# Kernel tuning notes

Measured on AMD Instinct MI355X. Metric: run time of the kernel, lower is better.

Reference implementation:

```python
import jax, jax.numpy as jnp
import numpy as np

B, L = 2, 256
CHAR, WORD = 8000, 50000
CE, WE, HID, REL = 128, 128, 256, 24
IN_DIM = CE + WE


def _lstm(x, mask, W, U, b):
    # Keras LSTM cell: z = x@W + h@U + b split into (i,f,g,o); masked steps carry state through.
    # x: (B, T, D) float, mask: (B, T) bool
    h0 = jnp.zeros((x.shape[0], U.shape[0]), x.dtype)

    def step(carry, xm):
        h, c = carry
        xt, mt = xm
        z = xt @ W + h @ U + b
        i, f, g, o = jnp.split(z, 4, axis=-1)
        c_new = jax.nn.sigmoid(f) * c + jax.nn.sigmoid(i) * jnp.tanh(g)
        h_new = jax.nn.sigmoid(o) * jnp.tanh(c_new)
        m = mt[:, None]
        h2 = jnp.where(m, h_new, h)
        c2 = jnp.where(m, c_new, c)
        return (h2, c2), h2

    _, hs = jax.lax.scan(step, (h0, h0), (jnp.swapaxes(x, 0, 1), jnp.swapaxes(mask, 0, 1)))
    return jnp.swapaxes(hs, 0, 1)  # (B, T, HID)


def _head(enc, Wu, bu, Wv, bv, Wuv, buv, Wc, bc):
    # Original: tile relu(u) over axis 1 (depends on j) and relu(v) over axis 2 (depends on i),
    # concat -> Dense. Equivalent fused form: split Wuv and broadcast-add the two projections.
    u = jax.nn.relu(enc @ Wu + bu)  # (B, L, E)
    v = jax.nn.relu(enc @ Wv + bv)  # (B, L, E)
    E = Wu.shape[1]
    uv = (jnp.einsum('bjd,de->bje', u, Wuv[:E])[:, None, :, :]
          + jnp.einsum('bid,de->bie', v, Wuv[E:])[:, :, None, :]
          + buv)  # (B, L, L, E)
    return uv @ Wc + bc  # (B, L, L, out)


def setup_inputs() -> dict:
    key = jax.random.key(0)
    ks = jax.random.split(key, 64)

    def w(k, shape):
        return jax.random.normal(k, shape, jnp.float32) * 0.05

    inp = {
        'inputs': jax.random.randint(ks[0], (B, L), 0, CHAR, jnp.int32),
        'input_words': jax.random.randint(ks[1], (B, L), 0, WORD, jnp.int32),
        'input_max_len': L,
        'embed_table': w(ks[2], (CHAR, CE)),
        'word_embed_table': w(ks[3], (WORD, WE)),
        'lstm_fwd_W': w(ks[4], (IN_DIM, 4 * HID)),
        'lstm_fwd_U': w(ks[5], (HID, 4 * HID)),
        'lstm_fwd_b': jnp.zeros((4 * HID,), jnp.float32),
        'lstm_bwd_W': w(ks[6], (IN_DIM, 4 * HID)),
        'lstm_bwd_U': w(ks[7], (HID, 4 * HID)),
        'lstm_bwd_b': jnp.zeros((4 * HID,), jnp.float32),
    }
    i = 8
    for name, out in (('eh', 1), ('hh', REL), ('tt', REL)):
        inp[f'{name}_u_W'] = w(ks[i], (2 * HID, CE)); i += 1
        inp[f'{name}_u_b'] = jnp.zeros((CE,), jnp.float32)
        inp[f'{name}_v_W'] = w(ks[i], (2 * HID, CE)); i += 1
        inp[f'{name}_v_b'] = jnp.zeros((CE,), jnp.float32)
        inp[f'{name}_uv_W'] = w(ks[i], (2 * CE, CE)); i += 1
        inp[f'{name}_uv_b'] = jnp.zeros((CE,), jnp.float32)
        inp[f'{name}_cls_W'] = w(ks[i], (CE, out)); i += 1
        inp[f'{name}_cls_b'] = jnp.zeros((out,), jnp.float32)
    return inp


def reference(inputs, input_words, input_max_len, embed_table, word_embed_table,
              lstm_fwd_W, lstm_fwd_U, lstm_fwd_b, lstm_bwd_W, lstm_bwd_U, lstm_bwd_b,
              eh_u_W, eh_u_b, eh_v_W, eh_v_b, eh_uv_W, eh_uv_b, eh_cls_W, eh_cls_b,
              hh_u_W, hh_u_b, hh_v_W, hh_v_b, hh_uv_W, hh_uv_b, hh_cls_W, hh_cls_b,
              tt_u_W, tt_u_b, tt_v_W, tt_v_b, tt_uv_W, tt_uv_b, tt_cls_W, tt_cls_b):
    mask = inputs != 0  # (B, L)
    x = jnp.concatenate([embed_table[inputs], word_embed_table[input_words]], axis=-1)
    h_fwd = _lstm(x, mask, lstm_fwd_W, lstm_fwd_U, lstm_fwd_b)
    h_bwd = _lstm(x[:, ::-1], mask[:, ::-1], lstm_bwd_W, lstm_bwd_U, lstm_bwd_b)[:, ::-1]
    enc = jnp.concatenate([h_fwd, h_bwd], axis=-1)  # (B, L, 2*HID)
    eh = jax.nn.sigmoid(_head(enc, eh_u_W, eh_u_b, eh_v_W, eh_v_b, eh_uv_W, eh_uv_b, eh_cls_W, eh_cls_b))
    hh = jax.nn.softmax(_head(enc, hh_u_W, hh_u_b, hh_v_W, hh_v_b, hh_uv_W, hh_uv_b, hh_cls_W, hh_cls_b), axis=-1)
    tt = jax.nn.softmax(_head(enc, tt_u_W, tt_u_b, tt_v_W, tt_v_b, tt_uv_W, tt_uv_b, tt_cls_W, tt_cls_b), axis=-1)
    return (eh, hh, tt)
```

## Files before the change

### kernel.cpp

```cpp
#include <hip/hip_runtime.h>
#include <hip/hip_bf16.h>

typedef unsigned short u16;
typedef unsigned int u32;
typedef unsigned long long u64;

#define LSEQ 256

constexpr int XW_F  = 0;
constexpr int XW_B  = 524288;
constexpr int HF_O  = 1048576;
constexpr int HB_O  = 1179648;
constexpr int PEH_O = 1703936;
constexpr int QEH_O = 1704448;
constexpr int PHH_O = 1704960;
constexpr int QHH_O = 1717248;
constexpr int PTT_O = 1729536;
constexpr int QTT_O = 1741824;

constexpr u64 SENT64 = 0x7FC000007FC00000ULL;

__device__ __forceinline__ float b2f(u16 u) {
  u32 x = ((u32)u) << 16; float f;
  __builtin_memcpy(&f, &x, 4); return f;
}
__device__ __forceinline__ u16 f2b(float f) {
  u32 x; __builtin_memcpy(&x, &f, 4);
  u32 r = (x + 0x7fffu + ((x >> 16) & 1u)) >> 16;
  return (u16)r;
}
__device__ __forceinline__ float sigm(float x) {
  return __builtin_amdgcn_rcpf(1.f + __expf(-x));
}
__device__ __forceinline__ float tanh_fast(float x) {
  return 2.f * __builtin_amdgcn_rcpf(1.f + __expf(-2.f * x)) - 1.f;
}
__device__ __forceinline__ u64 aload64(u64* p) {
  return __hip_atomic_load(p, __ATOMIC_RELAXED, __HIP_MEMORY_SCOPE_AGENT);
}
__device__ __forceinline__ void astore64(u64* p, u64 v) {
  __hip_atomic_store(p, v, __ATOMIC_RELAXED, __HIP_MEMORY_SCOPE_AGENT);
}
__device__ __forceinline__ bool detect_f32(const void* etab) {
  u32 w = ((const u32*)etab)[threadIdx.x & 63];
  u64 m = __ballot((w & 0x4000u) != 0);
  return __popcll(m) >= 16;
}
__device__ __forceinline__ float ldf(const void* p, int i, bool f32m) {
  return f32m ? ((const float*)p)[i] : b2f(((const u16*)p)[i]);
}

__global__ __launch_bounds__(256) void k_embed_xw(
    const int* __restrict__ toks, const int* __restrict__ wrds,
    const void* __restrict__ etab, const void* __restrict__ wtab,
    const void* __restrict__ Wf, const void* __restrict__ bf_,
    const void* __restrict__ Wb, const void* __restrict__ bb_,
    float* __restrict__ ws)
{
  __shared__ float xs[8][256];
  const int tid = threadIdx.x, bx = blockIdx.x;
  const int rg = bx >> 2, part = bx & 3, dir = part >> 1, ch = part & 1;
  {
    u64* hz = (u64*)(ws + HF_O) + (bx * 256 + tid) * 2;
    astore64(hz, SENT64); astore64(hz + 1, SENT64);
  }
  const bool f32m = detect_f32(etab);
  for (int rr = 0; rr < 8; rr++) {
    const int row = rg * 8 + rr;
    const int id = toks[row], wid = wrds[row];
    xs[rr][tid] = (tid < 128) ? ldf(etab, id * 128 + tid, f32m)
                              : ldf(wtab, wid * 128 + (tid - 128), f32m);
  }
  __syncthreads();
  const void* W = dir ? Wb : Wf;
  const void* bb = dir ? bb_ : bf_;
  const int c0 = ch * 512 + 2 * tid;
  float acc[8][2];
#pragma unroll
  for (int rr = 0; rr < 8; rr++) { acc[rr][0] = 0.f; acc[rr][1] = 0.f; }
  if (f32m) {
    const float2* W2 = (const float2*)W;
    for (int k = 0; k < 256; k++) {
      const float2 w = W2[k * 512 + (c0 >> 1)];
#pragma unroll
      for (int rr = 0; rr < 8; rr++) {
        const float x = xs[rr][k];
        acc[rr][0] = fmaf(x, w.x, acc[rr][0]);
        acc[rr][1] = fmaf(x, w.y, acc[rr][1]);
      }
    }
  } else {
    const u32* W2 = (const u32*)W;
    for (int k = 0; k < 256; k++) {
      const u32 v = W2[k * 512 + (c0 >> 1)];
      const float wx = b2f(v & 0xffff), wy = b2f(v >> 16);
#pragma unroll
      for (int rr = 0; rr < 8; rr++) {
        const float x = xs[rr][k];
        acc[rr][0] = fmaf(x, wx, acc[rr][0]);
        acc[rr][1] = fmaf(x, wy, acc[rr][1]);
      }
    }
  }
  const float b0 = ldf(bb, c0, f32m), b1 = ldf(bb, c0 + 1, f32m);
  float* xwb = ws + (dir ? XW_B : XW_F);
#pragma unroll
  for (int rr = 0; rr < 8; rr++) {
    const int row = rg * 8 + rr;
    float2 o = make_float2(acc[rr][0] + b0, acc[rr][1] + b1);
    *(float2*)(xwb + row * 1024 + c0) = o;
  }
}

__global__ __launch_bounds__(256, 1) void k_lstm(
    const int* __restrict__ toks,
    const void* __restrict__ Uf_raw, const void* __restrict__ Ub_raw,
    const void* __restrict__ etab, float* __restrict__ ws)
{
  __shared__ float2 hsh0[256], hsh1[256];
  __shared__ float psum0[8][128], psum1[8][128];
  __shared__ float zsh0[128], zsh1[128];
  __shared__ int msk[512];
  const int tid = threadIdx.x;
  const int w = blockIdx.x, base = w * 16;
  const int q = tid & 31, ksec = tid >> 5, k0 = ksec * 32;
  u64* h0 = (u64*)(ws + HF_O);
  u64* h1 = (u64*)(ws + HB_O);
  const float* xw0 = ws + XW_F;
  const float* xw1 = ws + XW_B;
  const bool f32m = detect_f32(etab);

  const int lc0 = 2 * q;
  const int gc0 = (lc0 >> 4) * 256 + base + (lc0 & 15);
  float2 us0[32], us1[32];
  if (f32m) {
    const float* U0 = (const float*)Uf_raw;
    const float* U1 = (const float*)Ub_raw;
#pragma unroll
    for (int j = 0; j < 32; j++) {
      us0[j] = *(const float2*)(U0 + (k0 + j) * 1024 + gc0);
      us1[j] = *(const float2*)(U1 + (k0 + j) * 1024 + gc0);
    }
  } else {
    const u32* U0 = (const u32*)Uf_raw;
    const u32* U1 = (const u32*)Ub_raw;
#pragma unroll
    for (int j = 0; j < 32; j++) {
      u32 v0 = U0[((k0 + j) * 1024 + gc0) >> 1];
      u32 v1 = U1[((k0 + j) * 1024 + gc0) >> 1];
      us0[j] = make_float2(b2f(v0 & 0xffff), b2f(v0 >> 16));
      us1[j] = make_float2(b2f(v1 & 0xffff), b2f(v1 >> 16));
    }
  }
  const int rlc = tid >> 1, rbb = tid & 1;
  const int rgc = (rlc >> 4) * 256 + base + (rlc & 15);
  const int gj = tid & 15, gb = (tid >> 4) & 1;
  const bool own = (tid >= base) && (tid < base + 16);

  msk[tid] = toks[tid]; msk[tid + 256] = toks[tid + 256];
  hsh0[tid] = make_float2(0.f, 0.f);
  hsh1[tid] = make_float2(0.f, 0.f);
  float c0Reg = 0.f, h0Reg = 0.f, c1Reg = 0.f, h1Reg = 0.f;
  float xw0reg = xw0[rbb * 262144 + 0 * 1024 + rgc];
  float xw1reg = xw1[rbb * 262144 + 255 * 1024 + rgc];
  __syncthreads();

  for (int s = 0; s < LSEQ; s++) {
    u64 v1 = 0;
    if (s > 0 && !own) v1 = aload64(&h1[(s - 1) * 256 + tid]);
    {
      float4 a = make_float4(0.f, 0.f, 0.f, 0.f);
#pragma unroll
      for (int j = 0; j < 32; j++) {
        const float2 h = hsh0[k0 + j];
        const float2 u = us0[j];
        a.x = fmaf(h.x, u.x, a.x); a.y = fmaf(h.y, u.x, a.y);
        a.z = fmaf(h.x, u.y, a.z); a.w = fmaf(h.y, u.y, a.w);
      }
      *(float4*)&psum0[ksec][4 * q] = a;
    }
    __syncthreads();
    if (tid < 128) {
      float z = xw0reg;
#pragma unroll
      for (int ks = 0; ks < 8; ks++) z += psum0[ks][tid];
      zsh0[tid] = z;
      const int t2 = (s < 255) ? s + 1 : 255;
      xw0reg = xw0[rbb * 262144 + t2 * 1024 + rgc];
    }
    __syncthreads();
    if (tid < 32) {
      const float zi = zsh0[gj * 2 + gb],        zf = zsh0[(16 + gj) * 2 + gb];
      const float zg = zsh0[(32 + gj) * 2 + gb], zo = zsh0[(48 + gj) * 2 + gb];
      const float cn = sigm(zf) * c0Reg + sigm(zi) * tanh_fast(zg);
      const float hn = sigm(zo) * tanh_fast(cn);
      if (msk[gb * 256 + s] != 0) { c0Reg = cn; h0Reg = hn; }
      const float hp = __shfl_xor(h0Reg, 16);
      if (tid < 16) {
        const float2 fv = make_float2(h0Reg, hp);
        hsh0[base + tid] = fv;
        u64 pv; __builtin_memcpy(&pv, &fv, 8);
        astore64(&h0[s * 256 + base + tid], pv);
      }
    }
    if (s > 0 && !own) {
      while (v1 == SENT64) v1 = aload64(&h1[(s - 1) * 256 + tid]);
      float2 hv; __builtin_memcpy(&hv, &v1, 8);
      hsh1[tid] = hv;
    }
    __syncthreads();
    u64 v0 = 0;
    if (s < 255 && !own) v0 = aload64(&h0[s * 256 + tid]);
    {
      float4 a = make_float4(0.f, 0.f, 0.f, 0.f);
#pragma unroll
      for (int j = 0; j < 32; j++) {
        const float2 h = hsh1[k0 + j];
        const float2 u = us1[j];
        a.x = fmaf(h.x, u.x, a.x); a.y = fmaf(h.y, u.x, a.y);
        a.z = fmaf(h.x, u.y, a.z); a.w = fmaf(h.y, u.y, a.w);
      }
      *(float4*)&psum1[ksec][4 * q] = a;
    }
    __syncthreads();
    if (tid < 128) {
      float z = xw1reg;
#pragma unroll
      for (int ks = 0; ks < 8; ks++) z += psum1[ks][tid];
      zsh1[tid] = z;
      const int t2 = (s < 255) ? 254 - s : 0;
      xw1reg = xw1[rbb * 262144 + t2 * 1024 + rgc];
    }
    __syncthreads();
    if (tid < 32) {
      const float zi = zsh1[gj * 2 + gb],        zf = zsh1[(16 + gj) * 2 + gb];
      const float zg = zsh1[(32 + gj) * 2 + gb], zo = zsh1[(48 + gj) * 2 + gb];
      const float cn = sigm(zf) * c1Reg + sigm(zi) * tanh_fast(zg);
      const float hn = sigm(zo) * tanh_fast(cn);
      if (msk[gb * 256 + (255 - s)] != 0) { c1Reg = cn; h1Reg = hn; }
      const float hp = __shfl_xor(h1Reg, 16);
      if (tid < 16) {
        const float2 fv = make_float2(h1Reg, hp);
        hsh1[base + tid] = fv;
        u64 pv; __builtin_memcpy(&pv, &fv, 8);
        astore64(&h1[s * 256 + base + tid], pv);
      }
    }
    if (s < 255 && !own) {
      while (v0 == SENT64) v0 = aload64(&h0[s * 256 + tid]);
      float2 hv; __builtin_memcpy(&hv, &v0, 8);
      hsh0[tid] = hv;
    }
    __syncthreads();
  }
}

struct HeadPack { const void* p[24]; };

__global__ __launch_bounds__(256) void k_uvpq(
    HeadPack pk, const void* __restrict__ etab, float* __restrict__ ws)
{
  __shared__ float encs_t[512][8];
  __shared__ float usv_t[2][128][8];
  __shared__ float apq[2][8][128];
  __shared__ float wc[3072];
  const int tid = threadIdx.x, rgp = blockIdx.x, hd = blockIdx.y;
  const bool f32m = detect_f32(etab);
  const void* uW  = pk.p[hd * 8 + 0]; const void* ub  = pk.p[hd * 8 + 1];
  const void* vW  = pk.p[hd * 8 + 2]; const void* vb  = pk.p[hd * 8 + 3];
  const void* uvW = pk.p[hd * 8 + 4]; const void* uvb = pk.p[hd * 8 + 5];
  const void* cW  = pk.p[hd * 8 + 6];
  const int nout = (hd == 0) ? 1 : 24;
  for (int i = tid; i < 128 * nout; i += 256) wc[i] = ldf(cW, i, f32m);
  for (int i = tid; i < 4096; i += 256) {
    const int h = i >> 3, rr = i & 7;
    const int row = rgp * 8 + rr, b = row >> 8, t = row & 255;
    encs_t[h][rr] = (h < 256)
        ? ws[HF_O + t * 512 + h * 2 + b]
        : ws[HB_O + (255 - t) * 512 + (h - 256) * 2 + b];
  }
  __syncthreads();
  {
    const int mat = tid >> 7, cs = tid & 127;
    const void* W = mat ? vW : uW;
    const float bias = ldf(mat ? vb : ub, cs, f32m);
    float acc[8];
#pragma unroll
    for (int rr = 0; rr < 8; rr++) acc[rr] = 0.f;
    if (f32m) {
      const float* Wf = (const float*)W;
      for (int k = 0; k < 512; k++) {
        const float wv = Wf[k * 128 + cs];
        const float4 e0 = *(const float4*)&encs_t[k][0];
        const float4 e1 = *(const float4*)&encs_t[k][4];
        acc[0] = fmaf(e0.x, wv, acc[0]); acc[1] = fmaf(e0.y, wv, acc[1]);
        acc[2] = fmaf(e0.z, wv, acc[2]); acc[3] = fmaf(e0.w, wv, acc[3]);
        acc[4] = fmaf(e1.x, wv, acc[4]); acc[5] = fmaf(e1.y, wv, acc[5]);
        acc[6] = fmaf(e1.z, wv, acc[6]); acc[7] = fmaf(e1.w, wv, acc[7]);
      }
    } else {
      const u16* Wf = (const u16*)W;
      for (int k = 0; k < 512; k++) {
        const float wv = b2f(Wf[k * 128 + cs]);
        const float4 e0 = *(const float4*)&encs_t[k][0];
        const float4 e1 = *(const float4*)&encs_t[k][4];
        acc[0] = fmaf(e0.x, wv, acc[0]); acc[1] = fmaf(e0.y, wv, acc[1]);
        acc[2] = fmaf(e0.z, wv, acc[2]); acc[3] = fmaf(e0.w, wv, acc[3]);
        acc[4] = fmaf(e1.x, wv, acc[4]); acc[5] = fmaf(e1.y, wv, acc[5]);
        acc[6] = fmaf(e1.z, wv, acc[6]); acc[7] = fmaf(e1.w, wv, acc[7]);
      }
    }
#pragma unroll
    for (int rr = 0; rr < 8; rr++)
      usv_t[mat][cs][rr] = fmaxf(acc[rr] + bias, 0.f);
  }
  __syncthreads();
  {
    const int half = tid >> 7, col = tid & 127;
    float acc[8];
#pragma unroll
    for (int rr = 0; rr < 8; rr++) acc[rr] = 0.f;
    if (f32m) {
      const float* Wf = (const float*)uvW;
      for (int k = 0; k < 128; k++) {
        const float wv = Wf[(half * 128 + k) * 128 + col];
        const float4 e0 = *(const float4*)&usv_t[half][k][0];
        const float4 e1 = *(const float4*)&usv_t[half][k][4];
        acc[0] = fmaf(e0.x, wv, acc[0]); acc[1] = fmaf(e0.y, wv, acc[1]);
        acc[2] = fmaf(e0.z, wv, acc[2]); acc[3] = fmaf(e0.w, wv, acc[3]);
        acc[4] = fmaf(e1.x, wv, acc[4]); acc[5] = fmaf(e1.y, wv, acc[5]);
        acc[6] = fmaf(e1.z, wv, acc[6]); acc[7] = fmaf(e1.w, wv, acc[7]);
      }
    } else {
      const u16* Wf = (const u16*)uvW;
      for (int k = 0; k < 128; k++) {
        const float wv = b2f(Wf[(half * 128 + k) * 128 + col]);
        const float4 e0 = *(const float4*)&usv_t[half][k][0];
        const float4 e1 = *(const float4*)&usv_t[half][k][4];
        acc[0] = fmaf(e0.x, wv, acc[0]); acc[1] = fmaf(e0.y, wv, acc[1]);
        acc[2] = fmaf(e0.z, wv, acc[2]); acc[3] = fmaf(e0.w, wv, acc[3]);
        acc[4] = fmaf(e1.x, wv, acc[4]); acc[5] = fmaf(e1.y, wv, acc[5]);
        acc[6] = fmaf(e1.z, wv, acc[6]); acc[7] = fmaf(e1.w, wv, acc[7]);
      }
    }
    const float bv = (half == 0) ? ldf(uvb, col, f32m) : 0.f;
#pragma unroll
    for (int rr = 0; rr < 8; rr++)
      apq[half][rr][col] = acc[rr] + bv;
  }
  __syncthreads();
  if (hd == 0) {
    if (tid < 16) {
      const int rr = tid >> 1, aq = tid & 1;
      float acc = 0.f;
      for (int e = 0; e < 128; e++) acc = fmaf(apq[aq][rr][e], wc[e], acc);
      const int row = rgp * 8 + rr;
      ws[(aq ? QEH_O : PEH_O) + row] = acc;
    }
  } else {
    const int PO = (hd == 1) ? PHH_O : PTT_O;
    const int QO = (hd == 1) ? QHH_O : QTT_O;
    for (int it = 0; it < 2; it++) {
      if (tid < 192) {
        const int task = it * 192 + tid;
        const int rr = task / 48, r2 = task % 48;
        const int aq = r2 / 24, o = r2 % 24;
        float acc = 0.f;
        for (int e = 0; e < 128; e++) acc = fmaf(apq[aq][rr][e], wc[e * 24 + o], acc);
        const int row = rgp * 8 + rr;
        ws[(aq ? QO : PO) + row * 24 + o] = acc;
      }
    }
  }
}

__global__ __launch_bounds__(256) void k_out(
    const void* __restrict__ bceh, const void* __restrict__ bchh,
    const void* __restrict__ bctt, const void* __restrict__ etab,
    const float* __restrict__ ws, void* __restrict__ outv)
{
  __shared__ float qh[24], qt[24];
  __shared__ float qe_s;
  __shared__ u32 sh[3072], st[3072];
  const bool f32m = detect_f32(etab);
  const int bi = blockIdx.x, b = bi >> 8, i = bi & 255;
  const int j = threadIdx.x;
  if (j < 24)       qh[j] = ws[QHH_O + (b * 256 + i) * 24 + j] + ldf(bchh, j, f32m);
  else if (j < 48)  qt[j - 24] = ws[QTT_O + (b * 256 + i) * 24 + (j - 24)] + ldf(bctt, j - 24, f32m);
  else if (j == 48) qe_s = ws[QEH_O + b * 256 + i] + ldf(bceh, 0, f32m);
  __syncthreads();
  {
    float v = ws[PEH_O + b * 256 + j] + qe_s;
    v = 1.f / (1.f + __expf(-v));
    if (f32m) ((float*)outv)[(b * 256 + i) * 256 + j] = v;
    else      ((u16*)outv)[(b * 256 + i) * 256 + j] = f2b(v);
  }
  float p[24];
  {
    const float* pp = ws + PHH_O + (b * 256 + j) * 24;
    float mx = -1e30f;
#pragma unroll
    for (int o = 0; o < 24; o++) { p[o] = pp[o] + qh[o]; mx = fmaxf(mx, p[o]); }
    float ssum = 0.f;
#pragma unroll
    for (int o = 0; o < 24; o++) { p[o] = __expf(p[o] - mx); ssum += p[o]; }
    const float inv = 1.f / ssum;
    if (f32m) {
      float* dst = (float*)outv + 131072 + (size_t)(bi * 256 + j) * 24;
#pragma unroll
      for (int m = 0; m < 6; m++)
        ((float4*)dst)[m] = make_float4(p[4*m]*inv, p[4*m+1]*inv, p[4*m+2]*inv, p[4*m+3]*inv);
    } else {
#pragma unroll
      for (int m = 0; m < 12; m++)
        sh[j * 12 + m] = ((u32)f2b(p[2*m+1] * inv) << 16) | (u32)f2b(p[2*m] * inv);
    }
  }
  {
    const float* pp = ws + PTT_O + (b * 256 + j) * 24;
    float mx = -1e30f;
#pragma unroll
    for (int o = 0; o < 24; o++) { p[o] = pp[o] + qt[o]; mx = fmaxf(mx, p[o]); }
    float ssum = 0.f;
#pragma unroll
    for (int o = 0; o < 24; o++) { p[o] = __expf(p[o] - mx); ssum += p[o]; }
    const float inv = 1.f / ssum;
    if (f32m) {
      float* dst = (float*)outv + 3276800 + (size_t)(bi * 256 + j) * 24;
#pragma unroll
      for (int m = 0; m < 6; m++)
        ((float4*)dst)[m] = make_float4(p[4*m]*inv, p[4*m+1]*inv, p[4*m+2]*inv, p[4*m+3]*inv);
    } else {
#pragma unroll
      for (int m = 0; m < 12; m++)
        st[j * 12 + m] = ((u32)f2b(p[2*m+1] * inv) << 16) | (u32)f2b(p[2*m] * inv);
    }
  }
  __syncthreads();
  if (!f32m) {
    u32* outu = (u32*)outv;
    const int baseH = 65536 + bi * 3072;
    const int baseT = 1638400 + bi * 3072;
#pragma unroll
    for (int m = 0; m < 12; m++) {
      outu[baseH + j + 256 * m] = sh[j + 256 * m];
      outu[baseT + j + 256 * m] = st[j + 256 * m];
    }
  }
}

extern "C" void kernel_launch(void* const* d_in, const int* in_sizes, int n_in,
                              void* d_out, int out_size, void* d_ws, size_t ws_size,
                              hipStream_t stream) {
  const int* toks = (const int*)d_in[0];
  const int* wrds = (const int*)d_in[1];
  float* ws = (float*)d_ws;

  k_embed_xw<<<dim3(256), dim3(256), 0, stream>>>(
      toks, wrds, d_in[3], d_in[4], d_in[5], d_in[7], d_in[8], d_in[10], ws);
  k_lstm<<<dim3(16), dim3(256), 0, stream>>>(toks, d_in[6], d_in[9], d_in[3], ws);
  HeadPack pk;
  for (int h = 0; h < 3; h++)
    for (int a = 0; a < 8; a++)
      pk.p[h * 8 + a] = d_in[11 + h * 8 + a];
  k_uvpq<<<dim3(64, 3), dim3(256), 0, stream>>>(pk, d_in[3], ws);
  k_out<<<dim3(512), dim3(256), 0, stream>>>(
      d_in[18], d_in[26], d_in[34], d_in[3], ws, d_out);
}
```

Baseline: 822.8 us.

## Run each LSTM direction/batch in one block with fp16 dot2 recurrence

Restructures the LSTM recurrence so each of four blocks owns one direction and one batch element. The whole U matrix is held as packed fp16 pairs, mostly in registers with the remainder in LDS, and the recurrent matvec uses fdot2. This removes the cross-block spin-wait exchange of hidden states through global memory, along with its sentinel initialisation, and cuts the barriers per step. The costs are lower recurrence precision from fp16 weights and state, very high register pressure from 384 packed registers per thread, and only four blocks running in parallel.

```diff
diff --git a/kernel.cpp b/kernel.cpp
--- a/kernel.cpp
+++ b/kernel.cpp
@@ -4,6 +4,7 @@
 typedef unsigned short u16;
 typedef unsigned int u32;
 typedef unsigned long long u64;
+typedef _Float16 half2v __attribute__((ext_vector_type(2)));
 
 #define LSEQ 256
 
@@ -18,8 +19,6 @@
 constexpr int PTT_O = 1729536;
 constexpr int QTT_O = 1741824;
 
-constexpr u64 SENT64 = 0x7FC000007FC00000ULL;
-
 __device__ __forceinline__ float b2f(u16 u) {
   u32 x = ((u32)u) << 16; float f;
   __builtin_memcpy(&f, &x, 4); return f;
@@ -35,12 +34,6 @@
 __device__ __forceinline__ float tanh_fast(float x) {
   return 2.f * __builtin_amdgcn_rcpf(1.f + __expf(-2.f * x)) - 1.f;
 }
-__device__ __forceinline__ u64 aload64(u64* p) {
-  return __hip_atomic_load(p, __ATOMIC_RELAXED, __HIP_MEMORY_SCOPE_AGENT);
-}
-__device__ __forceinline__ void astore64(u64* p, u64 v) {
-  __hip_atomic_store(p, v, __ATOMIC_RELAXED, __HIP_MEMORY_SCOPE_AGENT);
-}
 __device__ __forceinline__ bool detect_f32(const void* etab) {
   u32 w = ((const u32*)etab)[threadIdx.x & 63];
   u64 m = __ballot((w & 0x4000u) != 0);
@@ -48,6 +41,19 @@
 }
 __device__ __forceinline__ float ldf(const void* p, int i, bool f32m) {
   return f32m ? ((const float*)p)[i] : b2f(((const u16*)p)[i]);
+}
+__device__ __forceinline__ u32 packh(float lo, float hi) {
+  half2v v; v.x = (_Float16)lo; v.y = (_Float16)hi;
+  u32 r; __builtin_memcpy(&r, &v, 4); return r;
+}
+__device__ __forceinline__ float dot2f(u32 a, u32 b, float c) {
+  half2v av, bv;
+  __builtin_memcpy(&av, &a, 4); __builtin_memcpy(&bv, &b, 4);
+#if __has_builtin(__builtin_amdgcn_fdot2)
+  return __builtin_amdgcn_fdot2(av, bv, c, false);
+#else
+  return c + (float)av.x * (float)bv.x + (float)av.y * (float)bv.y;
+#endif
 }
 
 __global__ __launch_bounds__(256) void k_embed_xw(
@@ -60,10 +66,6 @@
   __shared__ float xs[8][256];
   const int tid = threadIdx.x, bx = blockIdx.x;
   const int rg = bx >> 2, part = bx & 3, dir = part >> 1, ch = part & 1;
-  {
-    u64* hz = (u64*)(ws + HF_O) + (bx * 256 + tid) * 2;
-    astore64(hz, SENT64); astore64(hz + 1, SENT64);
-  }
   const bool f32m = detect_f32(etab);
   for (int rr = 0; rr < 8; rr++) {
     const int row = rg * 8 + rr;
@@ -117,140 +119,88 @@
     const void* __restrict__ Uf_raw, const void* __restrict__ Ub_raw,
     const void* __restrict__ etab, float* __restrict__ ws)
 {
-  __shared__ float2 hsh0[256], hsh1[256];
-  __shared__ float psum0[8][128], psum1[8][128];
-  __shared__ float zsh0[128], zsh1[128];
-  __shared__ int msk[512];
+  __shared__ u32 ulds[32][1024];
+  __shared__ float zsh[1024];
+  __shared__ u32 hp[128];
+  __shared__ int msk[256];
   const int tid = threadIdx.x;
-  const int w = blockIdx.x, base = w * 16;
-  const int q = tid & 31, ksec = tid >> 5, k0 = ksec * 32;
-  u64* h0 = (u64*)(ws + HF_O);
-  u64* h1 = (u64*)(ws + HB_O);
-  const float* xw0 = ws + XW_F;
-  const float* xw1 = ws + XW_B;
+  const int dir = blockIdx.x >> 1, b = blockIdx.x & 1;
   const bool f32m = detect_f32(etab);
-
-  const int lc0 = 2 * q;
-  const int gc0 = (lc0 >> 4) * 256 + base + (lc0 & 15);
-  float2 us0[32], us1[32];
+  const void* Uraw = dir ? Ub_raw : Uf_raw;
+  const float* xw = ws + (dir ? XW_B : XW_F) + b * 262144;
+  float* hout = ws + (dir ? HB_O : HF_O);
+  const int c0 = 4 * tid;
+
+  u32 ur[96][4];
   if (f32m) {
-    const float* U0 = (const float*)Uf_raw;
-    const float* U1 = (const float*)Ub_raw;
-#pragma unroll
-    for (int j = 0; j < 32; j++) {
-      us0[j] = *(const float2*)(U0 + (k0 + j) * 1024 + gc0);
-      us1[j] = *(const float2*)(U1 + (k0 + j) * 1024 + gc0);
+    const float* U = (const float*)Uraw;
+#pragma unroll
+    for (int kp = 0; kp < 96; kp++) {
+      const float4 r0 = *(const float4*)(U + (2 * kp) * 1024 + c0);
+      const float4 r1 = *(const float4*)(U + (2 * kp + 1) * 1024 + c0);
+      ur[kp][0] = packh(r0.x, r1.x); ur[kp][1] = packh(r0.y, r1.y);
+      ur[kp][2] = packh(r0.z, r1.z); ur[kp][3] = packh(r0.w, r1.w);
+    }
+    for (int kp = 96; kp < 128; kp++) {
+      const float4 r0 = *(const float4*)(U + (2 * kp) * 1024 + c0);
+      const float4 r1 = *(const float4*)(U + (2 * kp + 1) * 1024 + c0);
+      ulds[kp - 96][c0]     = packh(r0.x, r1.x);
+      ulds[kp - 96][c0 + 1] = packh(r0.y, r1.y);
+      ulds[kp - 96][c0 + 2] = packh(r0.z, r1.z);
+      ulds[kp - 96][c0 + 3] = packh(r0.w, r1.w);
     }
   } else {
-    const u32* U0 = (const u32*)Uf_raw;
-    const u32* U1 = (const u32*)Ub_raw;
-#pragma unroll
-    for (int j = 0; j < 32; j++) {
-      u32 v0 = U0[((k0 + j) * 1024 + gc0) >> 1];
-      u32 v1 = U1[((k0 + j) * 1024 + gc0) >> 1];
-      us0[j] = make_float2(b2f(v0 & 0xffff), b2f(v0 >> 16));
-      us1[j] = make_float2(b2f(v1 & 0xffff), b2f(v1 >> 16));
-    }
-  }
-  const int rlc = tid >> 1, rbb = tid & 1;
-  const int rgc = (rlc >> 4) * 256 + base + (rlc & 15);
-  const int gj = tid & 15, gb = (tid >> 4) & 1;
-  const bool own = (tid >= base) && (tid < base + 16);
-
-  msk[tid] = toks[tid]; msk[tid + 256] = toks[tid + 256];
-  hsh0[tid] = make_float2(0.f, 0.f);
-  hsh1[tid] = make_float2(0.f, 0.f);
-  float c0Reg = 0.f, h0Reg = 0.f, c1Reg = 0.f, h1Reg = 0.f;
-  float xw0reg = xw0[rbb * 262144 + 0 * 1024 + rgc];
-  float xw1reg = xw1[rbb * 262144 + 255 * 1024 + rgc];
+    const u16* U = (const u16*)Uraw;
+#pragma unroll
+    for (int kp = 0; kp < 96; kp++) {
+      const ushort4 r0 = *(const ushort4*)(U + (2 * kp) * 1024 + c0);
+      const ushort4 r1 = *(const ushort4*)(U + (2 * kp + 1) * 1024 + c0);
+      ur[kp][0] = packh(b2f(r0.x), b2f(r1.x)); ur[kp][1] = packh(b2f(r0.y), b2f(r1.y));
+      ur[kp][2] = packh(b2f(r0.z), b2f(r1.z)); ur[kp][3] = packh(b2f(r0.w), b2f(r1.w));
+    }
+    for (int kp = 96; kp < 128; kp++) {
+      const ushort4 r0 = *(const ushort4*)(U + (2 * kp) * 1024 + c0);
+      const ushort4 r1 = *(const ushort4*)(U + (2 * kp + 1) * 1024 + c0);
+      ulds[kp - 96][c0]     = packh(b2f(r0.x), b2f(r1.x));
+      ulds[kp - 96][c0 + 1] = packh(b2f(r0.y), b2f(r1.y));
+      ulds[kp - 96][c0 + 2] = packh(b2f(r0.z), b2f(r1.z));
+      ulds[kp - 96][c0 + 3] = packh(b2f(r0.w), b2f(r1.w));
+    }
+  }
+  msk[tid] = toks[b * 256 + tid];
+  if (tid < 128) hp[tid] = 0u;
+  float cReg = 0.f, hReg = 0.f;
+  float4 xwv = *(const float4*)(xw + (dir ? 255 : 0) * 1024 + c0);
   __syncthreads();
 
   for (int s = 0; s < LSEQ; s++) {
-    u64 v1 = 0;
-    if (s > 0 && !own) v1 = aload64(&h1[(s - 1) * 256 + tid]);
-    {
-      float4 a = make_float4(0.f, 0.f, 0.f, 0.f);
-#pragma unroll
-      for (int j = 0; j < 32; j++) {
-        const float2 h = hsh0[k0 + j];
-        const float2 u = us0[j];
-        a.x = fmaf(h.x, u.x, a.x); a.y = fmaf(h.y, u.x, a.y);
-        a.z = fmaf(h.x, u.y, a.z); a.w = fmaf(h.y, u.y, a.w);
-      }
-      *(float4*)&psum0[ksec][4 * q] = a;
-    }
+    const int t = dir ? (255 - s) : s;
+    const int tn = dir ? (s < 255 ? 254 - s : 0) : (s < 255 ? s + 1 : 255);
+    float a0 = xwv.x, a1 = xwv.y, a2 = xwv.z, a3 = xwv.w;
+    const float4 xwn = *(const float4*)(xw + tn * 1024 + c0);
+#pragma unroll
+    for (int kp = 0; kp < 96; kp++) {
+      const u32 h2 = hp[kp];
+      a0 = dot2f(h2, ur[kp][0], a0); a1 = dot2f(h2, ur[kp][1], a1);
+      a2 = dot2f(h2, ur[kp][2], a2); a3 = dot2f(h2, ur[kp][3], a3);
+    }
+#pragma unroll
+    for (int kp = 0; kp < 32; kp++) {
+      const u32 h2 = hp[96 + kp];
+      const uint4 uu = *(const uint4*)&ulds[kp][c0];
+      a0 = dot2f(h2, uu.x, a0); a1 = dot2f(h2, uu.y, a1);
+      a2 = dot2f(h2, uu.z, a2); a3 = dot2f(h2, uu.w, a3);
+    }
+    zsh[c0] = a0; zsh[c0 + 1] = a1; zsh[c0 + 2] = a2; zsh[c0 + 3] = a3;
     __syncthreads();
-    if (tid < 128) {
-      float z = xw0reg;
-#pragma unroll
-      for (int ks = 0; ks < 8; ks++) z += psum0[ks][tid];
-      zsh0[tid] = z;
-      const int t2 = (s < 255) ? s + 1 : 255;
-      xw0reg = xw0[rbb * 262144 + t2 * 1024 + rgc];
-    }
-    __syncthreads();
-    if (tid < 32) {
-      const float zi = zsh0[gj * 2 + gb],        zf = zsh0[(16 + gj) * 2 + gb];
-      const float zg = zsh0[(32 + gj) * 2 + gb], zo = zsh0[(48 + gj) * 2 + gb];
-      const float cn = sigm(zf) * c0Reg + sigm(zi) * tanh_fast(zg);
-      const float hn = sigm(zo) * tanh_fast(cn);
-      if (msk[gb * 256 + s] != 0) { c0Reg = cn; h0Reg = hn; }
-      const float hp = __shfl_xor(h0Reg, 16);
-      if (tid < 16) {
-        const float2 fv = make_float2(h0Reg, hp);
-        hsh0[base + tid] = fv;
-        u64 pv; __builtin_memcpy(&pv, &fv, 8);
-        astore64(&h0[s * 256 + base + tid], pv);
-      }
-    }
-    if (s > 0 && !own) {
-      while (v1 == SENT64) v1 = aload64(&h1[(s - 1) * 256 + tid]);
-      float2 hv; __builtin_memcpy(&hv, &v1, 8);
-      hsh1[tid] = hv;
-    }
-    __syncthreads();
-    u64 v0 = 0;
-    if (s < 255 && !own) v0 = aload64(&h0[s * 256 + tid]);
-    {
-      float4 a = make_float4(0.f, 0.f, 0.f, 0.f);
-#pragma unroll
-      for (int j = 0; j < 32; j++) {
-        const float2 h = hsh1[k0 + j];
-        const float2 u = us1[j];
-        a.x = fmaf(h.x, u.x, a.x); a.y = fmaf(h.y, u.x, a.y);
-        a.z = fmaf(h.x, u.y, a.z); a.w = fmaf(h.y, u.y, a.w);
-      }
-      *(float4*)&psum1[ksec][4 * q] = a;
-    }
-    __syncthreads();
-    if (tid < 128) {
-      float z = xw1reg;
-#pragma unroll
-      for (int ks = 0; ks < 8; ks++) z += psum1[ks][tid];
-      zsh1[tid] = z;
-      const int t2 = (s < 255) ? 254 - s : 0;
-      xw1reg = xw1[rbb * 262144 + t2 * 1024 + rgc];
-    }
-    __syncthreads();
-    if (tid < 32) {
-      const float zi = zsh1[gj * 2 + gb],        zf = zsh1[(16 + gj) * 2 + gb];
-      const float zg = zsh1[(32 + gj) * 2 + gb], zo = zsh1[(48 + gj) * 2 + gb];
-      const float cn = sigm(zf) * c1Reg + sigm(zi) * tanh_fast(zg);
-      const float hn = sigm(zo) * tanh_fast(cn);
-      if (msk[gb * 256 + (255 - s)] != 0) { c1Reg = cn; h1Reg = hn; }
-      const float hp = __shfl_xor(h1Reg, 16);
-      if (tid < 16) {
-        const float2 fv = make_float2(h1Reg, hp);
-        hsh1[base + tid] = fv;
-        u64 pv; __builtin_memcpy(&pv, &fv, 8);
-        astore64(&h1[s * 256 + base + tid], pv);
-      }
-    }
-    if (s < 255 && !own) {
-      while (v0 == SENT64) v0 = aload64(&h0[s * 256 + tid]);
-      float2 hv; __builtin_memcpy(&hv, &v0, 8);
-      hsh0[tid] = hv;
-    }
+    const float zi = zsh[tid], zf = zsh[256 + tid];
+    const float zg = zsh[512 + tid], zo = zsh[768 + tid];
+    const float cn = sigm(zf) * cReg + sigm(zi) * tanh_fast(zg);
+    const float hn = sigm(zo) * tanh_fast(cn);
+    if (msk[t] != 0) { cReg = cn; hReg = hn; }
+    hout[t * 512 + tid * 2 + b] = hReg;
+    ((_Float16*)hp)[tid] = (_Float16)hReg;
+    xwv = xwn;
     __syncthreads();
   }
 }
@@ -277,7 +227,7 @@
     const int row = rgp * 8 + rr, b = row >> 8, t = row & 255;
     encs_t[h][rr] = (h < 256)
         ? ws[HF_O + t * 512 + h * 2 + b]
-        : ws[HB_O + (255 - t) * 512 + (h - 256) * 2 + b];
+        : ws[HB_O + t * 512 + (h - 256) * 2 + b];
   }
   __syncthreads();
   {
@@ -458,7 +408,7 @@
 
   k_embed_xw<<<dim3(256), dim3(256), 0, stream>>>(
       toks, wrds, d_in[3], d_in[4], d_in[5], d_in[7], d_in[8], d_in[10], ws);
-  k_lstm<<<dim3(16), dim3(256), 0, stream>>>(toks, d_in[6], d_in[9], d_in[3], ws);
+  k_lstm<<<dim3(4), dim3(256), 0, stream>>>(toks, d_in[6], d_in[9], d_in[3], ws);
   HeadPack pk;
   for (int h = 0; h < 3; h++)
     for (int a = 0; a < 8; a++)
```

Measured after the change: 1.117 ms. +35.7%, slower.
